# Performance work log

Measured on AMD Instinct MI355X. Metric: run time of the kernel, lower is better.

Reference implementation:

```python
import jax, jax.numpy as jnp
import numpy as np

NUM_EMBEDDINGS = 1024
EMBEDDING_DIM = 256

def setup_inputs() -> dict:
    key = jax.random.key(0)
    k1, k2 = jax.random.split(key)
    z_e = jax.random.normal(k1, (32, 256, 64, 64), dtype=jnp.float32)
    # nn.Embedding weight init uniform_(-1/K, 1/K)
    lim = 1.0 / NUM_EMBEDDINGS
    codebook = jax.random.uniform(k2, (NUM_EMBEDDINGS, EMBEDDING_DIM), dtype=jnp.float32,
                                  minval=-lim, maxval=lim)
    return {"z_e": z_e, "codebook": codebook}

def reference(z_e, codebook):
    B, C, H, W = z_e.shape
    # [B,C,H,W] -> [B*H*W, C]
    z_flat = jnp.transpose(z_e, (0, 2, 3, 1)).reshape(-1, C)
    # squared L2 distances: ||z||^2 + ||e||^2 - 2 z.e  -> [N, K]
    distances = (jnp.sum(z_flat ** 2, axis=1, keepdims=True)
                 + jnp.sum(codebook ** 2, axis=1)
                 - 2.0 * jnp.matmul(z_flat, codebook.T))
    encoding_indices = jnp.argmin(distances, axis=1)  # [N]
    z_q = codebook[encoding_indices].reshape(B, H, W, C)
    z_q = jnp.transpose(z_q, (0, 3, 1, 2))  # [B,C,H,W]
    sg = jax.lax.stop_gradient
    codebook_loss = jnp.mean((sg(z_q) - z_e) ** 2)
    commitment_loss = jnp.mean((sg(z_e) - z_q) ** 2)
    return z_q, codebook_loss + 0.25 * commitment_loss, encoding_indices
```

## Files before the change

### kernel.cpp

```cpp
#include <hip/hip_runtime.h>
#include <stdint.h>

typedef __attribute__((ext_vector_type(8))) _Float16 half8;
typedef __attribute__((ext_vector_type(4))) float f32x4;

#define CDIM 256
#define KCODES 1024
#define NPTS 131072
#define ZQ_ELEMS 33554432u
#define CAP 32768
#define MARGIN 3.0e-4f

#define WS_IMG 0
#define WS_S2 (16 * 65536)
#define WS_IDX (WS_S2 + 4096)
#define WS_PART (WS_IDX + NPTS * 4)
#define WS_CNT (WS_PART + 65536)
#define WS_LIST (WS_CNT + 64)

__device__ __forceinline__ float np_pairwise_sq_256(const float* x) {
    float res[2];
#pragma unroll
    for (int h = 0; h < 2; h++) {
        const float* a = x + h * 128;
        float r[8];
#pragma unroll
        for (int j = 0; j < 8; j++) r[j] = __fmul_rn(a[j], a[j]);
#pragma unroll
        for (int i = 8; i < 128; i += 8)
#pragma unroll
            for (int j = 0; j < 8; j++)
                r[j] = __fadd_rn(r[j], __fmul_rn(a[i + j], a[i + j]));
        res[h] = __fadd_rn(__fadd_rn(__fadd_rn(r[0], r[1]), __fadd_rn(r[2], r[3])),
                           __fadd_rn(__fadd_rn(r[4], r[5]), __fadd_rn(r[6], r[7])));
    }
    return __fadd_rn(res[0], res[1]);
}

__global__ __launch_bounds__(256) void vq_prep(const float* __restrict__ cb,
                                               unsigned char* __restrict__ img,
                                               int* __restrict__ cnt) {
    int t = threadIdx.x;
    if (blockIdx.x == 0 && t == 0) *cnt = 0;
    int codeLocal = t >> 5;
    int cg = t & 31;
    int k = blockIdx.x * 8 + codeLocal;
    const float* row = cb + k * CDIM + cg * 8;
    union H { _Float16 h[8]; uint4 u; } hi;
#pragma unroll
    for (int j = 0; j < 8; j++) hi.h[j] = (_Float16)(row[j] * 1024.f);
    int chunk = k >> 5, rowi = k & 31;
    int ks = cg >> 2, l4 = cg & 3;
    int q = rowi >> 4, l15 = rowi & 15;
    int lane = l4 * 16 + l15;
    *(uint4*)(img + chunk * 16384 + ((ks * 2 + q) << 10) + lane * 16) = hi.u;
}

__global__ __launch_bounds__(256) void vq_s2prep(const float* __restrict__ cb,
                                                 float* __restrict__ s2) {
    int k = blockIdx.x * 256 + threadIdx.x;
    float e[256];
#pragma unroll
    for (int c = 0; c < 256; c++) e[c] = cb[(size_t)k * CDIM + c];
    s2[k] = np_pairwise_sq_256(e);
}

__global__ __launch_bounds__(256, 3) void vq_dist(const float* __restrict__ z,
                                                  const unsigned char* __restrict__ img,
                                                  const float* __restrict__ s2g,
                                                  int* __restrict__ outIdx,
                                                  int* __restrict__ cnt,
                                                  int* __restrict__ list) {
    __shared__ __align__(16) unsigned char smem[2][16384];
    __shared__ float e2s[1024];
    int t = threadIdx.x;
    int lane = t & 63, wave = t >> 6;
    int l15 = lane & 15, l4 = lane >> 4;
    int blk0 = blockIdx.x * 128;
    int wbase = blk0 + wave * 32;
    int b = blk0 >> 12;
    int hwb0 = blk0 & 4095;
    const float* zb = z + (size_t)b * (CDIM * 4096);

#pragma unroll
    for (int i = 0; i < 4; i++) {
        size_t off = (size_t)(i * 256 + t) * 16;
        __builtin_amdgcn_global_load_lds(
            (const __attribute__((address_space(1))) void*)(img + off),
            (__attribute__((address_space(3))) void*)(&smem[0][0] + off), 16, 0, 0);
    }
#pragma unroll
    for (int i = 0; i < 4; i++) e2s[t + i * 256] = s2g[t + i * 256];

    half8 aHi[2][8];
#pragma unroll
    for (int ks = 0; ks < 8; ks++) {
        __syncthreads();
#pragma unroll
        for (int i = 0; i < 4; i++) {
            int u = i * 256 + t;
            int row = u >> 5, col4 = u & 31;
            const float* gsrc = zb + (size_t)(ks * 32 + row) * 4096 + hwb0 + col4 * 4;
            __builtin_amdgcn_global_load_lds(
                (const __attribute__((address_space(1))) void*)gsrc,
                (__attribute__((address_space(3))) void*)(&smem[1][0] + (size_t)u * 16), 16, 0, 0);
        }
        __syncthreads();
#pragma unroll
        for (int m = 0; m < 2; m++) {
            half8 h;
#pragma unroll
            for (int j = 0; j < 8; j++) {
                float f = *(const float*)(&smem[1][0] +
                        (size_t)(((l4 * 8 + j) * 128) + wave * 32 + m * 16 + l15) * 4) * 32.f;
                h[j] = (_Float16)f;
            }
            aHi[m][ks] = h;
        }
    }
    __syncthreads();

    float bestv[2][4], bestv2[2][4];
    int besti[2][4];
#pragma unroll
    for (int m = 0; m < 2; m++)
#pragma unroll
        for (int j = 0; j < 4; j++) { bestv[m][j] = 3.0e38f; bestv2[m][j] = 3.0e38f; besti[m][j] = 0; }

    int cur = 0;
    for (int chunk = 0; chunk < 32; chunk++) {
        if (chunk < 31) {
            const unsigned char* src = img + (size_t)(chunk + 1) * 16384;
            unsigned char* dst = &smem[cur ^ 1][0];
#pragma unroll
            for (int i = 0; i < 4; i++) {
                size_t off = (size_t)(i * 256 + t) * 16;
                __builtin_amdgcn_global_load_lds(
                    (const __attribute__((address_space(1))) void*)(src + off),
                    (__attribute__((address_space(3))) void*)(dst + off), 16, 0, 0);
            }
        }

        f32x4 acc[2][2];
#pragma unroll
        for (int m = 0; m < 2; m++)
#pragma unroll
            for (int q = 0; q < 2; q++) acc[m][q] = (f32x4){0.f, 0.f, 0.f, 0.f};

        const unsigned char* bufc = &smem[cur][0] + lane * 16;
#pragma unroll
        for (int ks = 0; ks < 8; ks++) {
            half8 b0 = *(const half8*)(bufc + (ks << 11));
            half8 b1 = *(const half8*)(bufc + (ks << 11) + 1024);
#pragma unroll
            for (int m = 0; m < 2; m++) {
                acc[m][0] = __builtin_amdgcn_mfma_f32_16x16x32_f16(aHi[m][ks], b0, acc[m][0], 0, 0, 0);
                acc[m][1] = __builtin_amdgcn_mfma_f32_16x16x32_f16(aHi[m][ks], b1, acc[m][1], 0, 0, 0);
            }
        }
#pragma unroll
        for (int q = 0; q < 2; q++) {
            int code = chunk * 32 + q * 16 + l15;
            float ev = e2s[code];
#pragma unroll
            for (int m = 0; m < 2; m++)
#pragma unroll
                for (int j = 0; j < 4; j++) {
                    float s = fmaf(acc[m][q][j], -6.103515625e-05f, ev);
                    if (s < bestv[m][j]) { bestv2[m][j] = bestv[m][j]; bestv[m][j] = s; besti[m][j] = code; }
                    else if (s < bestv2[m][j]) bestv2[m][j] = s;
                }
        }
        __syncthreads();
        cur ^= 1;
    }

#pragma unroll
    for (int m = 0; m < 2; m++)
#pragma unroll
        for (int j = 0; j < 4; j++) {
            float v = bestv[m][j], v2 = bestv2[m][j];
            int idx = besti[m][j];
#pragma unroll
            for (int off = 1; off < 16; off <<= 1) {
                float ov = __shfl_xor(v, off);
                float ov2 = __shfl_xor(v2, off);
                int oi = __shfl_xor(idx, off);
                if (ov < v || (ov == v && oi < idx)) { v2 = fminf(v, ov2); v = ov; idx = oi; }
                else v2 = fminf(v2, ov);
            }
            if (l15 == 0) {
                int p = wbase + m * 16 + l4 * 4 + j;
                outIdx[p] = idx;
                if (v2 - v < MARGIN) {
                    int pos = atomicAdd(cnt, 1);
                    if (pos < CAP) list[pos] = p;
                }
            }
        }
}

__global__ __launch_bounds__(256) void vq_cbt(const float* __restrict__ cb,
                                              float* __restrict__ cbT) {
    int k = blockIdx.x * 256 + threadIdx.x;
    for (int c = 0; c < 256; c++) cbT[c * 1024 + k] = cb[(size_t)k * 256 + c];
}

__global__ __launch_bounds__(256) void vq_rescue(const float* __restrict__ z,
                                                 const float* __restrict__ cbT,
                                                 const float* __restrict__ s2,
                                                 const int* __restrict__ list,
                                                 const int* __restrict__ cnt,
                                                 int* __restrict__ outIdx) {
    __shared__ float zs[8][256];
    __shared__ float S1s[8];
    __shared__ float rv[256];
    __shared__ int ri[256];
    int n = *cnt; if (n > CAP) n = CAP;
    int t = threadIdx.x;
    for (int base = blockIdx.x * 8; base < n; base += gridDim.x * 8) {
        int npts = n - base; if (npts > 8) npts = 8;
        __syncthreads();
        {
            int pp = t >> 5, c0 = (t & 31) * 8;
            if (pp < npts) {
                int p = list[base + pp];
                int b = p >> 12, hw = p & 4095;
                const float* zp = z + ((size_t)b << 20) + hw;
#pragma unroll
                for (int j = 0; j < 8; j++) zs[pp][c0 + j] = zp[(size_t)(c0 + j) << 12];
            }
        }
        __syncthreads();
        if (t < npts) S1s[t] = np_pairwise_sq_256(zs[t]);
        __syncthreads();

        float d[8][4];
#pragma unroll
        for (int pp = 0; pp < 8; pp++)
#pragma unroll
            for (int q = 0; q < 4; q++) d[pp][q] = 0.f;
        for (int c = 0; c < 256; c++) {
            const float* er = cbT + c * 1024 + t;
            float e0 = er[0], e1 = er[256], e2v = er[512], e3 = er[768];
#pragma unroll
            for (int pp = 0; pp < 8; pp++) {
                float zc = zs[pp][c];
                d[pp][0] = fmaf(zc, e0, d[pp][0]);
                d[pp][1] = fmaf(zc, e1, d[pp][1]);
                d[pp][2] = fmaf(zc, e2v, d[pp][2]);
                d[pp][3] = fmaf(zc, e3, d[pp][3]);
            }
        }
        float s2v[4] = {s2[t], s2[256 + t], s2[512 + t], s2[768 + t]};

        float bv[8]; int bi[8];
#pragma unroll
        for (int pp = 0; pp < 8; pp++) {
            float v = 3.4e38f; int i0 = 0;
#pragma unroll
            for (int q = 0; q < 4; q++) {
                float dist = __fsub_rn(__fadd_rn(S1s[pp], s2v[q]), __fmul_rn(2.0f, d[pp][q]));
                if (dist < v) { v = dist; i0 = q * 256 + t; }
            }
            bv[pp] = v; bi[pp] = i0;
        }
        for (int pp = 0; pp < 8; pp++) {
            if (pp >= npts) break;
            rv[t] = bv[pp]; ri[t] = bi[pp];
            __syncthreads();
            for (int sft = 128; sft > 0; sft >>= 1) {
                if (t < sft) {
                    if (rv[t + sft] < rv[t] || (rv[t + sft] == rv[t] && ri[t + sft] < ri[t])) {
                        rv[t] = rv[t + sft]; ri[t] = ri[t + sft];
                    }
                }
                __syncthreads();
            }
            if (t == 0) outIdx[list[base + pp]] = ri[0];
            __syncthreads();
        }
    }
}

__global__ __launch_bounds__(256) void vq_gather(const float* __restrict__ z,
                                                 const float* __restrict__ cb,
                                                 const int* __restrict__ idxs,
                                                 float* __restrict__ out,
                                                 float* __restrict__ partial) {
    int tid = blockIdx.x * 256 + threadIdx.x;
    int hw = tid & 4095;
    int bg = tid >> 12;
    int b = bg >> 5, cg = bg & 31;
    int id = idxs[(b << 12) + hw];
    const float4* cr = (const float4*)(cb + (size_t)id * CDIM + cg * 8);
    float4 v0 = cr[0], v1 = cr[1];
    float va[8] = {v0.x, v0.y, v0.z, v0.w, v1.x, v1.y, v1.z, v1.w};
    size_t base = ((size_t)(b * 256 + cg * 8) << 12) + hw;
    float s = 0.f;
#pragma unroll
    for (int j = 0; j < 8; j++) {
        float ze = z[base + ((size_t)j << 12)];
        out[base + ((size_t)j << 12)] = va[j];
        float d = va[j] - ze;
        s = fmaf(d, d, s);
    }
    if (cg == 0) out[(size_t)ZQ_ELEMS + 1u + (b << 12) + hw] = (float)id;
#pragma unroll
    for (int off = 32; off > 0; off >>= 1) s += __shfl_down(s, off);
    __shared__ float red[4];
    if ((threadIdx.x & 63) == 0) red[threadIdx.x >> 6] = s;
    __syncthreads();
    if (threadIdx.x == 0) partial[blockIdx.x] = red[0] + red[1] + red[2] + red[3];
}

__global__ __launch_bounds__(512) void vq_finalize(const float* __restrict__ partial,
                                                   float* __restrict__ out) {
    int t = threadIdx.x;
    double s = 0.0;
    for (int i = t; i < 16384; i += 512) s += (double)partial[i];
#pragma unroll
    for (int off = 32; off > 0; off >>= 1) s += __shfl_down(s, off);
    __shared__ double sd[8];
    if ((t & 63) == 0) sd[t >> 6] = s;
    __syncthreads();
    if (t == 0) {
        double tot = sd[0] + sd[1] + sd[2] + sd[3] + sd[4] + sd[5] + sd[6] + sd[7];
        out[ZQ_ELEMS] = (float)(1.25 * tot / (double)ZQ_ELEMS);
    }
}

extern "C" void kernel_launch(void* const* d_in, const int* in_sizes, int n_in,
                              void* d_out, int out_size, void* d_ws, size_t ws_size,
                              hipStream_t stream) {
    const float* z = (const float*)d_in[0];
    const float* cb = (const float*)d_in[1];
    unsigned char* ws = (unsigned char*)d_ws;
    unsigned char* img = ws + WS_IMG;
    float* cbT = (float*)(ws + WS_IMG);
    float* s2 = (float*)(ws + WS_S2);
    int* idx = (int*)(ws + WS_IDX);
    float* partial = (float*)(ws + WS_PART);
    int* cnt = (int*)(ws + WS_CNT);
    int* list = (int*)(ws + WS_LIST);
    float* out = (float*)d_out;

    vq_prep<<<128, 256, 0, stream>>>(cb, img, cnt);
    vq_s2prep<<<4, 256, 0, stream>>>(cb, s2);
    vq_dist<<<1024, 256, 0, stream>>>(z, img, s2, idx, cnt, list);
    vq_cbt<<<4, 256, 0, stream>>>(cb, cbT);
    vq_rescue<<<512, 256, 0, stream>>>(z, cbT, s2, list, cnt, idx);
    vq_gather<<<16384, 256, 0, stream>>>(z, cb, idx, out, partial);
    vq_finalize<<<1, 512, 0, stream>>>(partial, out);
}
```

Before: 372.2 us.

## Stage fp16 z fragments in LDS and double block size in VQ distance kernel

The distance kernel now uses 512-thread blocks covering 256 points each. The converted fp16 z fragments are stored in a 128 KB LDS region instead of being held in registers. Each streamed codebook chunk is therefore reused across twice as many points, halving codebook reads from L2. The per-chunk barrier is replaced by an explicit vmcnt wait plus s_barrier, and codebook norms are read from global memory instead of an LDS copy. The trade-off is extra LDS reads of the A operand for every MFMA and much lower occupancy, since the roughly 160 KB of LDS allows only one block per CU.

```diff
diff --git a/kernel.cpp b/kernel.cpp
--- a/kernel.cpp
+++ b/kernel.cpp
@@ -65,60 +65,58 @@
     s2[k] = np_pairwise_sq_256(e);
 }
 
-__global__ __launch_bounds__(256, 3) void vq_dist(const float* __restrict__ z,
+__global__ __launch_bounds__(512, 2) void vq_dist(const float* __restrict__ z,
                                                   const unsigned char* __restrict__ img,
                                                   const float* __restrict__ s2g,
                                                   int* __restrict__ outIdx,
                                                   int* __restrict__ cnt,
                                                   int* __restrict__ list) {
-    __shared__ __align__(16) unsigned char smem[2][16384];
-    __shared__ float e2s[1024];
+    __shared__ __align__(16) unsigned char alds[131072];
+    __shared__ __align__(16) unsigned char cbuf[2][16384];
     int t = threadIdx.x;
     int lane = t & 63, wave = t >> 6;
     int l15 = lane & 15, l4 = lane >> 4;
-    int blk0 = blockIdx.x * 128;
+    int blk0 = blockIdx.x * 256;
     int wbase = blk0 + wave * 32;
     int b = blk0 >> 12;
     int hwb0 = blk0 & 4095;
     const float* zb = z + (size_t)b * (CDIM * 4096);
-
-#pragma unroll
-    for (int i = 0; i < 4; i++) {
-        size_t off = (size_t)(i * 256 + t) * 16;
+    unsigned char* sbase = &cbuf[0][0];
+
+#pragma unroll
+    for (int ks = 0; ks < 8; ks++) {
+        __syncthreads();
+#pragma unroll
+        for (int i = 0; i < 4; i++) {
+            int u = i * 512 + t;
+            int row = u >> 6, col16 = u & 63;
+            const float* gsrc = zb + (size_t)(ks * 32 + row) * 4096 + hwb0 + col16 * 4;
+            __builtin_amdgcn_global_load_lds(
+                (const __attribute__((address_space(1))) void*)gsrc,
+                (__attribute__((address_space(3))) void*)(sbase + (size_t)u * 16), 16, 0, 0);
+        }
+        __syncthreads();
+#pragma unroll
+        for (int m = 0; m < 2; m++) {
+            union H { _Float16 h[8]; uint4 u; } hv;
+#pragma unroll
+            for (int j = 0; j < 8; j++) {
+                float f = *(const float*)(sbase +
+                        (size_t)(((l4 * 8 + j) << 8) + wave * 32 + m * 16 + l15) * 4) * 32.f;
+                hv.h[j] = (_Float16)f;
+            }
+            *(uint4*)(alds + (((size_t)((wave * 2 + m) * 8 + ks)) << 10) + lane * 16) = hv.u;
+        }
+    }
+    __syncthreads();
+
+#pragma unroll
+    for (int i = 0; i < 2; i++) {
+        size_t off = (size_t)(i * 512 + t) * 16;
         __builtin_amdgcn_global_load_lds(
             (const __attribute__((address_space(1))) void*)(img + off),
-            (__attribute__((address_space(3))) void*)(&smem[0][0] + off), 16, 0, 0);
-    }
-#pragma unroll
-    for (int i = 0; i < 4; i++) e2s[t + i * 256] = s2g[t + i * 256];
-
-    half8 aHi[2][8];
-#pragma unroll
-    for (int ks = 0; ks < 8; ks++) {
-        __syncthreads();
-#pragma unroll
-        for (int i = 0; i < 4; i++) {
-            int u = i * 256 + t;
-            int row = u >> 5, col4 = u & 31;
-            const float* gsrc = zb + (size_t)(ks * 32 + row) * 4096 + hwb0 + col4 * 4;
-            __builtin_amdgcn_global_load_lds(
-                (const __attribute__((address_space(1))) void*)gsrc,
-                (__attribute__((address_space(3))) void*)(&smem[1][0] + (size_t)u * 16), 16, 0, 0);
-        }
-        __syncthreads();
-#pragma unroll
-        for (int m = 0; m < 2; m++) {
-            half8 h;
-#pragma unroll
-            for (int j = 0; j < 8; j++) {
-                float f = *(const float*)(&smem[1][0] +
-                        (size_t)(((l4 * 8 + j) * 128) + wave * 32 + m * 16 + l15) * 4) * 32.f;
-                h[j] = (_Float16)f;
-            }
-            aHi[m][ks] = h;
-        }
-    }
-    __syncthreads();
+            (__attribute__((address_space(3))) void*)(&cbuf[0][0] + off), 16, 0, 0);
+    }
 
     float bestv[2][4], bestv2[2][4];
     int besti[2][4];
@@ -127,19 +125,25 @@
 #pragma unroll
         for (int j = 0; j < 4; j++) { bestv[m][j] = 3.0e38f; bestv2[m][j] = 3.0e38f; besti[m][j] = 0; }
 
-    int cur = 0;
+    const unsigned char* ba = alds + lane * 16;
     for (int chunk = 0; chunk < 32; chunk++) {
-        if (chunk < 31) {
+        int cur = chunk & 1;
+        asm volatile("s_waitcnt vmcnt(0)" ::: "memory");
+        __builtin_amdgcn_s_barrier();
+
+        if (chunk + 1 < 32) {
             const unsigned char* src = img + (size_t)(chunk + 1) * 16384;
-            unsigned char* dst = &smem[cur ^ 1][0];
-#pragma unroll
-            for (int i = 0; i < 4; i++) {
-                size_t off = (size_t)(i * 256 + t) * 16;
+            unsigned char* dst = &cbuf[cur ^ 1][0];
+#pragma unroll
+            for (int i = 0; i < 2; i++) {
+                size_t off = (size_t)(i * 512 + t) * 16;
                 __builtin_amdgcn_global_load_lds(
                     (const __attribute__((address_space(1))) void*)(src + off),
                     (__attribute__((address_space(3))) void*)(dst + off), 16, 0, 0);
             }
         }
+        float ev0 = s2g[chunk * 32 + l15];
+        float ev1 = s2g[chunk * 32 + 16 + l15];
 
         f32x4 acc[2][2];
 #pragma unroll
@@ -147,21 +151,22 @@
 #pragma unroll
             for (int q = 0; q < 2; q++) acc[m][q] = (f32x4){0.f, 0.f, 0.f, 0.f};
 
-        const unsigned char* bufc = &smem[cur][0] + lane * 16;
+        const unsigned char* bb = &cbuf[cur][0] + lane * 16;
 #pragma unroll
         for (int ks = 0; ks < 8; ks++) {
-            half8 b0 = *(const half8*)(bufc + (ks << 11));
-            half8 b1 = *(const half8*)(bufc + (ks << 11) + 1024);
+            half8 b0 = *(const half8*)(bb + (ks << 11));
+            half8 b1 = *(const half8*)(bb + (ks << 11) + 1024);
 #pragma unroll
             for (int m = 0; m < 2; m++) {
-                acc[m][0] = __builtin_amdgcn_mfma_f32_16x16x32_f16(aHi[m][ks], b0, acc[m][0], 0, 0, 0);
-                acc[m][1] = __builtin_amdgcn_mfma_f32_16x16x32_f16(aHi[m][ks], b1, acc[m][1], 0, 0, 0);
+                half8 am = *(const half8*)(ba + (((size_t)((wave * 2 + m) * 8 + ks)) << 10));
+                acc[m][0] = __builtin_amdgcn_mfma_f32_16x16x32_f16(am, b0, acc[m][0], 0, 0, 0);
+                acc[m][1] = __builtin_amdgcn_mfma_f32_16x16x32_f16(am, b1, acc[m][1], 0, 0, 0);
             }
         }
 #pragma unroll
         for (int q = 0; q < 2; q++) {
             int code = chunk * 32 + q * 16 + l15;
-            float ev = e2s[code];
+            float ev = q ? ev1 : ev0;
 #pragma unroll
             for (int m = 0; m < 2; m++)
 #pragma unroll
@@ -171,8 +176,6 @@
                     else if (s < bestv2[m][j]) bestv2[m][j] = s;
                 }
         }
-        __syncthreads();
-        cur ^= 1;
     }
 
 #pragma unroll
@@ -347,7 +350,7 @@
 
     vq_prep<<<128, 256, 0, stream>>>(cb, img, cnt);
     vq_s2prep<<<4, 256, 0, stream>>>(cb, s2);
-    vq_dist<<<1024, 256, 0, stream>>>(z, img, s2, idx, cnt, list);
+    vq_dist<<<512, 512, 0, stream>>>(z, img, s2, idx, cnt, list);
     vq_cbt<<<4, 256, 0, stream>>>(cb, cbT);
     vq_rescue<<<512, 256, 0, stream>>>(z, cbT, s2, list, cnt, idx);
     vq_gather<<<16384, 256, 0, stream>>>(z, cb, idx, out, partial);
```

Result: slower. 384.5 us (+3.3%).
